# Kernel tuning notes

Measured on AMD Instinct MI355X. Metric: run time of the kernel, lower is better.

## Reference

```python
import jax, jax.numpy as jnp
import numpy as np

B, S, D, U = 32, 2048, 1024, 1024


def setup_inputs() -> dict:
    key = jax.random.key(0)
    ks = jax.random.split(key, 7)
    scale = 1.0 / np.sqrt(D)
    return {
        "query": jax.random.normal(ks[0], (B, D), dtype=jnp.float32),
        "values": jax.random.normal(ks[1], (B, S, D), dtype=jnp.float32),
        "w1": jax.random.normal(ks[2], (D, U), dtype=jnp.float32) * scale,
        "b1": jnp.zeros((U,), dtype=jnp.float32),
        "w2": jax.random.normal(ks[3], (D, U), dtype=jnp.float32) * scale,
        "b2": jnp.zeros((U,), dtype=jnp.float32),
        "wv": jax.random.normal(ks[4], (U, 1), dtype=jnp.float32) * (1.0 / np.sqrt(U)),
        "bv": jnp.zeros((1,), dtype=jnp.float32),
    }


def reference(query, values, w1, b1, w2, b2, wv, bv):
    # q_proj: [B, 1, U]; v_proj: [B, S, U]
    q_proj = (query @ w1 + b1)[:, None, :]
    v_proj = jnp.einsum("bsd,du->bsu", values, w2) + b2
    # score: [B, S, 1]
    score = jnp.tanh(q_proj + v_proj) @ wv + bv
    attention_weights = jax.nn.softmax(score, axis=1)  # softmax over seq axis
    context_vector = jnp.sum(attention_weights * values, axis=1)  # [B, D]
    return (context_vector, attention_weights)
```

## Files before the change

kernel.cpp:

```cpp
#include <hip/hip_runtime.h>
#include <hip/hip_bf16.h>

#define BB 32
#define SS 2048
#define DD 1024
#define UU 1024
#define MBLK 64

typedef short bf16x8 __attribute__((ext_vector_type(8)));
typedef float f32x4 __attribute__((ext_vector_type(4)));
typedef int i32x4 __attribute__((ext_vector_type(4)));
typedef unsigned int u32;

__device__ __forceinline__ unsigned short f2bf(float x) {
    union { float f; unsigned int u; } v; v.f = x;
    unsigned int r = v.u + 0x7fffu + ((v.u >> 16) & 1u);
    return (unsigned short)(r >> 16);
}

__device__ __forceinline__ f32x4 ntload4(const float* p) {
    return __builtin_nontemporal_load(reinterpret_cast<const f32x4*>(p));
}

__device__ __forceinline__ u32 cvtpk(float lo, float hi) {
    u32 r;
    asm("v_cvt_pk_bf16_f32 %0, %1, %2" : "=v"(r) : "v"(lo), "v"(hi));
    return r;
}

__global__ void zero_kernel(float* __restrict__ qp2) {
    qp2[blockIdx.x * 256 + threadIdx.x] = 0.f;
}

__global__ void qproj_kernel(const float* __restrict__ query, const float* __restrict__ w1,
                             const float* __restrict__ b1, const float* __restrict__ b2,
                             float* __restrict__ qp2) {
    __shared__ float qs[4][128];
    const int uc = blockIdx.x;
    const int bg = blockIdx.y;
    const int ds = blockIdx.z;
    const int t = threadIdx.x;
    if (t < 128) {
#pragma unroll
        for (int bi = 0; bi < 4; ++bi)
            qs[bi][t] = query[(bg * 4 + bi) * DD + ds * 128 + t];
    }
    __syncthreads();
    const int u = uc * 256 + t;
    float a0 = 0.f, a1 = 0.f, a2 = 0.f, a3 = 0.f;
    const float* wp = w1 + (size_t)(ds * 128) * UU + u;
#pragma unroll 4
    for (int d = 0; d < 128; ++d) {
        const float w = wp[(size_t)d * UU];
        a0 = fmaf(qs[0][d], w, a0);
        a1 = fmaf(qs[1][d], w, a1);
        a2 = fmaf(qs[2][d], w, a2);
        a3 = fmaf(qs[3][d], w, a3);
    }
    const float bb = (ds == 0) ? (b1[u] + b2[u]) : 0.f;
    atomicAdd(&qp2[(bg * 4 + 0) * UU + u], a0 + bb);
    atomicAdd(&qp2[(bg * 4 + 1) * UU + u], a1 + bb);
    atomicAdd(&qp2[(bg * 4 + 2) * UU + u], a2 + bb);
    atomicAdd(&qp2[(bg * 4 + 3) * UU + u], a3 + bb);
}

__global__ void w2q_kernel(const float* __restrict__ w2, unsigned short* __restrict__ w2q) {
    __shared__ float tile[64][65];
    const int k0 = (blockIdx.x >> 4) * 64;
    const int u0 = (blockIdx.x & 15) * 64;
    const int t = threadIdx.x;
    {
        const int kr = t >> 2, uc = (t & 3) * 16;
        const float* src = w2 + (size_t)(k0 + kr) * UU + u0 + uc;
#pragma unroll
        for (int j = 0; j < 4; ++j) {
            f32x4 v = *reinterpret_cast<const f32x4*>(src + j * 4);
            tile[kr][uc + j * 4 + 0] = v[0]; tile[kr][uc + j * 4 + 1] = v[1];
            tile[kr][uc + j * 4 + 2] = v[2]; tile[kr][uc + j * 4 + 3] = v[3];
        }
    }
    __syncthreads();
    const int c = t >> 5;
    const int uqL = c >> 1, ksL = c & 1;
    const int uq = (u0 >> 4) + uqL, ks = (k0 >> 5) + ksL;
#pragma unroll
    for (int li = 0; li < 2; ++li) {
        const int l = (t & 31) * 2 + li;
        const int colL = uqL * 16 + (l & 15);
        const int kL = ksL * 32 + (l >> 4) * 8;
        bf16x8 pk;
#pragma unroll
        for (int e = 0; e < 8; ++e) pk[e] = (short)f2bf(tile[kL + e][colL]);
        *reinterpret_cast<bf16x8*>(&w2q[(size_t)(((uq * 32 + ks) * 64 + l)) * 8]) = pk;
    }
}

__global__ __launch_bounds__(512, 2)
void score_kernel(const float* __restrict__ values, const unsigned short* __restrict__ w2q,
                  const float* __restrict__ qp2, const float* __restrict__ wv,
                  const float* __restrict__ bv, float* __restrict__ score) {
    __shared__ __align__(16) unsigned short Apk[MBLK * DD];
    __shared__ float ssum[8][MBLK];

    const int blk = blockIdx.x;
    const int b = blk >> 5;
    const int s0 = (blk & 31) * MBLK;
    const int tid = threadIdx.x;
    const int lane = tid & 63;
    const int wid = tid >> 6;
    const int arow = lane & 15;

    const int row = tid >> 3;
    const int g = tid & 7;
    const int q = g & 3;
    const int lsw = ((row & 15) + 16 * q) ^ q;
    const float* src = values + ((size_t)b * SS + s0 + row) * DD + g * 8;
    unsigned short* sdst = Apk + (size_t)(g >> 2) * 2048 + (size_t)(row >> 4) * 512 + lsw * 8;

#define STAGE_W(j, x, y)                                                   \
    {                                                                      \
        u32 q0 = cvtpk((x)[0], (x)[1]), q1 = cvtpk((x)[2], (x)[3]);        \
        u32 q2 = cvtpk((y)[0], (y)[1]), q3 = cvtpk((y)[2], (y)[3]);        \
        i32x4 w_ = {(int)q0, (int)q1, (int)q2, (int)q3};                   \
        *reinterpret_cast<i32x4*>(sdst + (size_t)(j) * 4096) = w_;         \
    }

    const unsigned short* Ab = Apk + (size_t)(lane ^ ((lane >> 4) & 3)) * 8;
    const unsigned short* wqs =
        w2q + ((size_t)__builtin_amdgcn_readfirstlane(wid) << 16);
    const size_t lane8 = (size_t)lane * 8;

    f32x4 acc0[4][4], acc1[4][4];
#pragma unroll
    for (int mf = 0; mf < 4; ++mf)
#pragma unroll
        for (int nf = 0; nf < 4; ++nf) {
            f32x4 z = {0.f, 0.f, 0.f, 0.f};
            acc0[mf][nf] = z; acc1[mf][nf] = z;
        }

    {
        f32x4 x0 = ntload4(src), y0 = ntload4(src + 4);
        f32x4 x1 = ntload4(src + 64), y1 = ntload4(src + 68);
        STAGE_W(0, x0, y0);
        STAGE_W(1, x1, y1);
    }
    __syncthreads();

#pragma unroll 1
    for (int p = 0; p < 8; ++p) {
        f32x4 L0, L1, L2, L3;
        if (p < 7) {
            const float* s1 = src + (2 * p + 2) * 64;
            const float* s2 = src + (2 * p + 3) * 64;
            L0 = ntload4(s1); L1 = ntload4(s1 + 4);
            L2 = ntload4(s2); L3 = ntload4(s2 + 4);
        }
#pragma unroll
        for (int kk = 0; kk < 4; ++kk) {
            const int ks = p * 4 + kk;
            bf16x8 aF[4];
#pragma unroll
            for (int mf = 0; mf < 4; ++mf)
                aF[mf] = *reinterpret_cast<const bf16x8*>(Ab + ((size_t)(ks * 4 + mf) << 9));
            bf16x8 b0[4], b1[4];
#pragma unroll
            for (int nf = 0; nf < 4; ++nf) {
                b0[nf] = *reinterpret_cast<const bf16x8*>(
                    wqs + (((size_t)(nf * 32 + ks)) << 9) + lane8);
                b1[nf] = *reinterpret_cast<const bf16x8*>(
                    wqs + (((size_t)((nf + 32) * 32 + ks)) << 9) + lane8);
            }
#pragma unroll
            for (int mf = 0; mf < 4; ++mf)
#pragma unroll
                for (int nf = 0; nf < 4; ++nf)
                    acc0[mf][nf] = __builtin_amdgcn_mfma_f32_16x16x32_bf16(
                        aF[mf], b0[nf], acc0[mf][nf], 0, 0, 0);
#pragma unroll
            for (int mf = 0; mf < 4; ++mf)
#pragma unroll
                for (int nf = 0; nf < 4; ++nf)
                    acc1[mf][nf] = __builtin_amdgcn_mfma_f32_16x16x32_bf16(
                        aF[mf], b1[nf], acc1[mf][nf], 0, 0, 0);
        }
        if (p < 7) {
            STAGE_W(2 * p + 2, L0, L1);
            STAGE_W(2 * p + 3, L2, L3);
            __syncthreads();
        }
    }
#undef STAGE_W

    float rowsum[16];
#pragma unroll
    for (int i = 0; i < 16; ++i) rowsum[i] = 0.f;
#pragma unroll
    for (int nf = 0; nf < 4; ++nf) {
        const int u0a = (wid * 4 + nf) * 16 + arow;
        const int u1a = (32 + wid * 4 + nf) * 16 + arow;
        const float qv0 = qp2[b * UU + u0a], wv0 = wv[u0a];
        const float qv1 = qp2[b * UU + u1a], wv1 = wv[u1a];
#pragma unroll
        for (int mf = 0; mf < 4; ++mf)
#pragma unroll
            for (int i = 0; i < 4; ++i) {
                float h0 = acc0[mf][nf][i] + qv0;
                float e0 = __expf(2.f * h0);
                rowsum[mf * 4 + i] = fmaf(1.f - 2.f / (e0 + 1.f), wv0, rowsum[mf * 4 + i]);
                float h1 = acc1[mf][nf][i] + qv1;
                float e1 = __expf(2.f * h1);
                rowsum[mf * 4 + i] = fmaf(1.f - 2.f / (e1 + 1.f), wv1, rowsum[mf * 4 + i]);
            }
    }
#pragma unroll
    for (int i = 0; i < 16; ++i) {
        float v = rowsum[i];
        v += __shfl_xor(v, 1);
        v += __shfl_xor(v, 2);
        v += __shfl_xor(v, 4);
        v += __shfl_xor(v, 8);
        rowsum[i] = v;
    }
    if ((lane & 15) == 0) {
        const int rg = lane >> 4;
#pragma unroll
        for (int mf = 0; mf < 4; ++mf)
#pragma unroll
            for (int i = 0; i < 4; ++i)
                ssum[wid][mf * 16 + rg * 4 + i] = rowsum[mf * 4 + i];
    }
    __syncthreads();
    if (tid < MBLK) {
        float sc = bv[0];
#pragma unroll
        for (int w = 0; w < 8; ++w) sc += ssum[w][tid];
        score[b * SS + s0 + tid] = sc;
    }
}

__global__ void softmax_kernel(const float* __restrict__ score, float* __restrict__ weights) {
    __shared__ float red[8];
    const int b = blockIdx.x;
    const int t = threadIdx.x;
    float local[8];
    float mx = -1e30f;
#pragma unroll
    for (int i = 0; i < 8; ++i) {
        local[i] = score[b * SS + i * 256 + t];
        mx = fmaxf(mx, local[i]);
    }
    for (int off = 1; off < 64; off <<= 1) mx = fmaxf(mx, __shfl_xor(mx, off));
    if ((t & 63) == 0) red[t >> 6] = mx;
    __syncthreads();
    const float m = fmaxf(fmaxf(red[0], red[1]), fmaxf(red[2], red[3]));
    float sum = 0.f;
#pragma unroll
    for (int i = 0; i < 8; ++i) {
        local[i] = __expf(local[i] - m);
        sum += local[i];
    }
    for (int off = 1; off < 64; off <<= 1) sum += __shfl_xor(sum, off);
    if ((t & 63) == 0) red[4 + (t >> 6)] = sum;
    __syncthreads();
    const float inv = 1.f / (red[4] + red[5] + red[6] + red[7]);
#pragma unroll
    for (int i = 0; i < 8; ++i) weights[b * SS + i * 256 + t] = local[i] * inv;
}

__global__ void context_kernel(const float* __restrict__ values, const float* __restrict__ weights,
                               float* __restrict__ ctx) {
    __shared__ float ws[SS];
    __shared__ f32x4 red[16][16];
    const int b = blockIdx.x;
    const int dc = blockIdx.y;
    const int t = threadIdx.x;
    for (int i = t; i < SS; i += 256) ws[i] = weights[b * SS + i];
    __syncthreads();
    const int dt = t & 15;
    const int ph = t >> 4;
    const int d = dc * 64 + dt * 4;
    const float* vb = values + (size_t)b * SS * DD + d;
    f32x4 acc = {0.f, 0.f, 0.f, 0.f};
#pragma unroll 8
    for (int s = ph; s < SS; s += 16) {
        const float w = ws[s];
        f32x4 v = ntload4(vb + (size_t)s * DD);
        acc[0] = fmaf(w, v[0], acc[0]);
        acc[1] = fmaf(w, v[1], acc[1]);
        acc[2] = fmaf(w, v[2], acc[2]);
        acc[3] = fmaf(w, v[3], acc[3]);
    }
    red[ph][dt] = acc;
    __syncthreads();
    if (t < 16) {
        f32x4 r = red[0][t];
#pragma unroll
        for (int w = 1; w < 16; ++w) {
            f32x4 x = red[w][t];
#pragma unroll
            for (int i = 0; i < 4; ++i) r[i] += x[i];
        }
        *reinterpret_cast<f32x4*>(ctx + (size_t)b * DD + dc * 64 + t * 4) = r;
    }
}

extern "C" void kernel_launch(void* const* d_in, const int* in_sizes, int n_in,
                              void* d_out, int out_size, void* d_ws, size_t ws_size,
                              hipStream_t stream) {
    const float* query  = (const float*)d_in[0];
    const float* values = (const float*)d_in[1];
    const float* w1     = (const float*)d_in[2];
    const float* b1     = (const float*)d_in[3];
    const float* w2     = (const float*)d_in[4];
    const float* b2     = (const float*)d_in[5];
    const float* wv     = (const float*)d_in[6];
    const float* bv     = (const float*)d_in[7];

    float* ctx     = (float*)d_out;
    float* weights = (float*)d_out + (size_t)BB * DD;

    float* qp2           = (float*)d_ws;
    unsigned short* w2q  = (unsigned short*)((char*)d_ws + 131072);
    float* score         = (float*)((char*)d_ws + 131072 + 2097152);

    zero_kernel<<<dim3(BB * UU / 256), 256, 0, stream>>>(qp2);
    qproj_kernel<<<dim3(4, 8, 8), 256, 0, stream>>>(query, w1, b1, b2, qp2);
    w2q_kernel<<<dim3(256), 256, 0, stream>>>(w2, w2q);
    score_kernel<<<dim3(BB * SS / MBLK), 512, 0, stream>>>(values, w2q, qp2, wv, bv, score);
    softmax_kernel<<<dim3(BB), 256, 0, stream>>>(score, weights);
    context_kernel<<<dim3(BB, 16), 256, 0, stream>>>(values, weights, ctx);
}
```

Baseline: 246.5 us.

## Split score kernel across 16 waves, each owning 64 U columns

Doubles the score kernel block from 512 to 1024 threads (16 waves). Each wave now computes one 64-column slice of U instead of two, halving the per-wave accumulators and B-fragment loads. The values staging loop is re-laid out so 16 threads cover a 128-float chunk per row per stage. The aim is more latency hiding and lower register pressure, at the cost of fewer A-fragment reuses per wave and a larger cross-wave reduction.

```diff
diff --git a/kernel.cpp b/kernel.cpp
--- a/kernel.cpp
+++ b/kernel.cpp
@@ -95,12 +95,12 @@
     }
 }
 
-__global__ __launch_bounds__(512, 2)
+__global__ __launch_bounds__(1024, 4)
 void score_kernel(const float* __restrict__ values, const unsigned short* __restrict__ w2q,
                   const float* __restrict__ qp2, const float* __restrict__ wv,
                   const float* __restrict__ bv, float* __restrict__ score) {
     __shared__ __align__(16) unsigned short Apk[MBLK * DD];
-    __shared__ float ssum[8][MBLK];
+    __shared__ float ssum[16][MBLK];
 
     const int blk = blockIdx.x;
     const int b = blk >> 5;
@@ -109,20 +109,21 @@
     const int lane = tid & 63;
     const int wid = tid >> 6;
     const int arow = lane & 15;
-
-    const int row = tid >> 3;
-    const int g = tid & 7;
+    const int uq0 = wid * 4;
+
+    const int row = tid >> 4;
+    const int g = tid & 15;
     const int q = g & 3;
     const int lsw = ((row & 15) + 16 * q) ^ q;
     const float* src = values + ((size_t)b * SS + s0 + row) * DD + g * 8;
     unsigned short* sdst = Apk + (size_t)(g >> 2) * 2048 + (size_t)(row >> 4) * 512 + lsw * 8;
 
-#define STAGE_W(j, x, y)                                                   \
+#define STAGE_W(p, x, y)                                                   \
     {                                                                      \
         u32 q0 = cvtpk((x)[0], (x)[1]), q1 = cvtpk((x)[2], (x)[3]);        \
         u32 q2 = cvtpk((y)[0], (y)[1]), q3 = cvtpk((y)[2], (y)[3]);        \
         i32x4 w_ = {(int)q0, (int)q1, (int)q2, (int)q3};                   \
-        *reinterpret_cast<i32x4*>(sdst + (size_t)(j) * 4096) = w_;         \
+        *reinterpret_cast<i32x4*>(sdst + (size_t)(p) * 8192) = w_;         \
     }
 
     const unsigned short* Ab = Apk + (size_t)(lane ^ ((lane >> 4) & 3)) * 8;
@@ -130,31 +131,25 @@
         w2q + ((size_t)__builtin_amdgcn_readfirstlane(wid) << 16);
     const size_t lane8 = (size_t)lane * 8;
 
-    f32x4 acc0[4][4], acc1[4][4];
+    f32x4 acc[4][4];
 #pragma unroll
     for (int mf = 0; mf < 4; ++mf)
 #pragma unroll
-        for (int nf = 0; nf < 4; ++nf) {
-            f32x4 z = {0.f, 0.f, 0.f, 0.f};
-            acc0[mf][nf] = z; acc1[mf][nf] = z;
-        }
+        for (int nf = 0; nf < 4; ++nf) { f32x4 z = {0.f, 0.f, 0.f, 0.f}; acc[mf][nf] = z; }
 
     {
         f32x4 x0 = ntload4(src), y0 = ntload4(src + 4);
-        f32x4 x1 = ntload4(src + 64), y1 = ntload4(src + 68);
         STAGE_W(0, x0, y0);
-        STAGE_W(1, x1, y1);
     }
     __syncthreads();
 
 #pragma unroll 1
     for (int p = 0; p < 8; ++p) {
-        f32x4 L0, L1, L2, L3;
+        f32x4 L0, L1;
         if (p < 7) {
-            const float* s1 = src + (2 * p + 2) * 64;
-            const float* s2 = src + (2 * p + 3) * 64;
-            L0 = ntload4(s1); L1 = ntload4(s1 + 4);
-            L2 = ntload4(s2); L3 = ntload4(s2 + 4);
+            const float* s1 = src + (p + 1) * 128;
+            L0 = ntload4(s1);
+            L1 = ntload4(s1 + 4);
         }
 #pragma unroll
         for (int kk = 0; kk < 4; ++kk) {
@@ -163,30 +158,20 @@
 #pragma unroll
             for (int mf = 0; mf < 4; ++mf)
                 aF[mf] = *reinterpret_cast<const bf16x8*>(Ab + ((size_t)(ks * 4 + mf) << 9));
-            bf16x8 b0[4], b1[4];
-#pragma unroll
-            for (int nf = 0; nf < 4; ++nf) {
-                b0[nf] = *reinterpret_cast<const bf16x8*>(
+            bf16x8 bF[4];
+#pragma unroll
+            for (int nf = 0; nf < 4; ++nf)
+                bF[nf] = *reinterpret_cast<const bf16x8*>(
                     wqs + (((size_t)(nf * 32 + ks)) << 9) + lane8);
-                b1[nf] = *reinterpret_cast<const bf16x8*>(
-                    wqs + (((size_t)((nf + 32) * 32 + ks)) << 9) + lane8);
-            }
 #pragma unroll
             for (int mf = 0; mf < 4; ++mf)
 #pragma unroll
                 for (int nf = 0; nf < 4; ++nf)
-                    acc0[mf][nf] = __builtin_amdgcn_mfma_f32_16x16x32_bf16(
-                        aF[mf], b0[nf], acc0[mf][nf], 0, 0, 0);
-#pragma unroll
-            for (int mf = 0; mf < 4; ++mf)
-#pragma unroll
-                for (int nf = 0; nf < 4; ++nf)
-                    acc1[mf][nf] = __builtin_amdgcn_mfma_f32_16x16x32_bf16(
-                        aF[mf], b1[nf], acc1[mf][nf], 0, 0, 0);
+                    acc[mf][nf] = __builtin_amdgcn_mfma_f32_16x16x32_bf16(
+                        aF[mf], bF[nf], acc[mf][nf], 0, 0, 0);
         }
         if (p < 7) {
-            STAGE_W(2 * p + 2, L0, L1);
-            STAGE_W(2 * p + 3, L2, L3);
+            STAGE_W(p + 1, L0, L1);
             __syncthreads();
         }
     }
@@ -197,20 +182,17 @@
     for (int i = 0; i < 16; ++i) rowsum[i] = 0.f;
 #pragma unroll
     for (int nf = 0; nf < 4; ++nf) {
-        const int u0a = (wid * 4 + nf) * 16 + arow;
-        const int u1a = (32 + wid * 4 + nf) * 16 + arow;
-        const float qv0 = qp2[b * UU + u0a], wv0 = wv[u0a];
-        const float qv1 = qp2[b * UU + u1a], wv1 = wv[u1a];
+        const int u = (uq0 + nf) * 16 + arow;
+        const float qv = qp2[b * UU + u];
+        const float wvv = wv[u];
 #pragma unroll
         for (int mf = 0; mf < 4; ++mf)
 #pragma unroll
             for (int i = 0; i < 4; ++i) {
-                float h0 = acc0[mf][nf][i] + qv0;
-                float e0 = __expf(2.f * h0);
-                rowsum[mf * 4 + i] = fmaf(1.f - 2.f / (e0 + 1.f), wv0, rowsum[mf * 4 + i]);
-                float h1 = acc1[mf][nf][i] + qv1;
-                float e1 = __expf(2.f * h1);
-                rowsum[mf * 4 + i] = fmaf(1.f - 2.f / (e1 + 1.f), wv1, rowsum[mf * 4 + i]);
+                float h = acc[mf][nf][i] + qv;
+                float e = __expf(2.f * h);
+                float th = 1.f - 2.f / (e + 1.f);
+                rowsum[mf * 4 + i] = fmaf(th, wvv, rowsum[mf * 4 + i]);
             }
     }
 #pragma unroll
@@ -234,7 +216,7 @@
     if (tid < MBLK) {
         float sc = bv[0];
 #pragma unroll
-        for (int w = 0; w < 8; ++w) sc += ssum[w][tid];
+        for (int w = 0; w < 16; ++w) sc += ssum[w][tid];
         score[b * SS + s0 + tid] = sc;
     }
 }
@@ -327,7 +309,7 @@
     zero_kernel<<<dim3(BB * UU / 256), 256, 0, stream>>>(qp2);
     qproj_kernel<<<dim3(4, 8, 8), 256, 0, stream>>>(query, w1, b1, b2, qp2);
     w2q_kernel<<<dim3(256), 256, 0, stream>>>(w2, w2q);
-    score_kernel<<<dim3(BB * SS / MBLK), 512, 0, stream>>>(values, w2q, qp2, wv, bv, score);
+    score_kernel<<<dim3(BB * SS / MBLK), 1024, 0, stream>>>(values, w2q, qp2, wv, bv, score);
     softmax_kernel<<<dim3(BB), 256, 0, stream>>>(score, weights);
     context_kernel<<<dim3(BB, 16), 256, 0, stream>>>(values, weights, ctx);
 }
```

Measured after the change: 239.5 us. -2.8%, faster.
